# Kernel tuning notes

Measured on AMD Instinct MI355X. Metric: run time of the kernel, lower is better.

## Reference

```python
import jax, jax.numpy as jnp
import numpy as np

N = 100000
E = 1600000
D_IN, D_HID, D_OUT = 256, 256, 128


def _sage_conv(x, src, dst, Wl, bl, Wr, n_nodes):
    # PyG SAGEConv (aggr='mean'): out = lin_l(mean_{j in N(i)} x_j) + lin_r(x_i)
    msg = x[src]                                               # [E, d]
    summed = jax.ops.segment_sum(msg, dst, num_segments=n_nodes)  # [N, d]
    deg = jax.ops.segment_sum(jnp.ones((src.shape[0],), x.dtype), dst,
                              num_segments=n_nodes)            # [N]
    agg = summed / jnp.maximum(deg, 1.0)[:, None]              # mean, 0 if isolated
    return agg @ Wl.T + bl + x @ Wr.T


def setup_inputs() -> dict:
    key = jax.random.key(0)
    ks = jax.random.split(key, 8)
    x = jax.random.normal(ks[0], (N, D_IN), dtype=jnp.float32)
    edge_index = jax.random.randint(ks[1], (2, E), 0, N, dtype=jnp.int32)
    s1 = 1.0 / np.sqrt(D_IN)
    s2 = 1.0 / np.sqrt(D_HID)
    W1l = jax.random.uniform(ks[2], (D_HID, D_IN), jnp.float32, -s1, s1)
    b1 = jnp.zeros((D_HID,), jnp.float32)
    W1r = jax.random.uniform(ks[3], (D_HID, D_IN), jnp.float32, -s1, s1)
    W2l = jax.random.uniform(ks[4], (D_OUT, D_HID), jnp.float32, -s2, s2)
    b2 = jnp.zeros((D_OUT,), jnp.float32)
    W2r = jax.random.uniform(ks[5], (D_OUT, D_HID), jnp.float32, -s2, s2)
    return {"x": x, "edge_index": edge_index, "W1l": W1l, "b1": b1,
            "W1r": W1r, "W2l": W2l, "b2": b2, "W2r": W2r}


def reference(x, edge_index, W1l, b1, W1r, W2l, b2, W2r):
    src, dst = edge_index[0], edge_index[1]
    h = _sage_conv(x, src, dst, W1l, b1, W1r, x.shape[0])
    h = jax.nn.relu(h)
    out = _sage_conv(h, src, dst, W2l, b2, W2r, x.shape[0])
    return out
```

## Files before the change

kernel.cpp:

```cpp
#include <hip/hip_runtime.h>

#define DK 256
#define BN 256
#define NBLK 512

typedef __attribute__((ext_vector_type(8))) short bf16x8;
typedef __attribute__((ext_vector_type(4))) float f32x4;

__device__ __forceinline__ unsigned short f2b(float f) {
    unsigned u = __builtin_bit_cast(unsigned, f);
    u += 0x7FFFu + ((u >> 16) & 1u);
    return (unsigned short)(u >> 16);
}
__device__ __forceinline__ float b2f(unsigned short s) {
    return __builtin_bit_cast(float, (unsigned)s << 16);
}
__device__ __forceinline__ void gld_lds16(void* lds, const void* g) {
    __builtin_amdgcn_global_load_lds(
        (const __attribute__((address_space(1))) unsigned int*)g,
        (__attribute__((address_space(3))) unsigned int*)lds, 16, 0, 0);
}

__global__ __launch_bounds__(256) void k_cvt(const float* __restrict__ src,
                                             unsigned short* __restrict__ dst, int n4) {
    int i = blockIdx.x * 256 + threadIdx.x;
    if (i < n4) {
        float4 v = reinterpret_cast<const float4*>(src)[i];
        ushort4 o = make_ushort4(f2b(v.x), f2b(v.y), f2b(v.z), f2b(v.w));
        reinterpret_cast<ushort4*>(dst)[i] = o;
    }
}

__global__ __launch_bounds__(256) void k_cvtw(const float* __restrict__ a,
                                              const float* __restrict__ b,
                                              const float* __restrict__ c,
                                              const float* __restrict__ d,
                                              unsigned short* __restrict__ Wb1,
                                              unsigned short* __restrict__ Wb2) {
    int i = blockIdx.x * 256 + threadIdx.x;
    const float* s;
    unsigned short* o;
    if (i < 16384)      { s = a; o = Wb1; }
    else if (i < 32768) { s = b; o = Wb1 + 256 * 256; i -= 16384; }
    else if (i < 40960) { s = c; o = Wb2;             i -= 32768; }
    else                { s = d; o = Wb2 + 128 * 256; i -= 40960; }
    float4 v = reinterpret_cast<const float4*>(s)[i];
    ushort4 w = make_ushort4(f2b(v.x), f2b(v.y), f2b(v.z), f2b(v.w));
    reinterpret_cast<ushort4*>(o)[i] = w;
}

__global__ __launch_bounds__(256) void k_scan_a(const int* __restrict__ in,
                                                int* __restrict__ bsum, int N) {
    __shared__ int sm[256];
    int t = threadIdx.x;
    int i0 = blockIdx.x * 1024 + t * 4;
    int s = 0;
    if (i0 + 3 < N) {
        int4 v = *reinterpret_cast<const int4*>(in + i0);
        s = v.x + v.y + v.z + v.w;
    } else {
        for (int i = i0; i < min(i0 + 4, N); ++i) s += in[i];
    }
    sm[t] = s;
    __syncthreads();
    for (int off = 128; off > 0; off >>= 1) {
        if (t < off) sm[t] += sm[t + off];
        __syncthreads();
    }
    if (t == 0) bsum[blockIdx.x] = sm[0];
}

__global__ __launch_bounds__(256) void k_scan_b(const int* __restrict__ bsum,
                                                int* __restrict__ boff,
                                                int* __restrict__ totN, int NB) {
    __shared__ int sm[256];
    int t = threadIdx.x;
    sm[t] = (t < NB) ? bsum[t] : 0;
    __syncthreads();
    for (int off = 1; off < 256; off <<= 1) {
        int v = (t >= off) ? sm[t - off] : 0;
        __syncthreads();
        sm[t] += v;
        __syncthreads();
    }
    if (t < NB) boff[t] = (t == 0) ? 0 : sm[t - 1];
    if (t == NB - 1) *totN = sm[t];
}

__global__ __launch_bounds__(256) void k_scan_c(const int* __restrict__ in,
                                                const int* __restrict__ boff,
                                                int* __restrict__ rowptr,
                                                float* __restrict__ invdeg, int N) {
    __shared__ int sm[256];
    int t = threadIdx.x;
    int i0 = blockIdx.x * 1024 + t * 4;
    int d0 = 0, d1 = 0, d2 = 0, d3 = 0;
    if (i0 + 3 < N) {
        int4 v = *reinterpret_cast<const int4*>(in + i0);
        d0 = v.x; d1 = v.y; d2 = v.z; d3 = v.w;
    } else {
        if (i0 + 0 < N) d0 = in[i0 + 0];
        if (i0 + 1 < N) d1 = in[i0 + 1];
        if (i0 + 2 < N) d2 = in[i0 + 2];
        if (i0 + 3 < N) d3 = in[i0 + 3];
    }
    int s = d0 + d1 + d2 + d3;
    sm[t] = s;
    __syncthreads();
    for (int off = 1; off < 256; off <<= 1) {
        int v = (t >= off) ? sm[t - off] : 0;
        __syncthreads();
        sm[t] += v;
        __syncthreads();
    }
    int run = boff[blockIdx.x] + sm[t] - s;
    int dd[4] = {d0, d1, d2, d3};
#pragma unroll
    for (int i = 0; i < 4; ++i) {
        int idx = i0 + i;
        if (idx < N) {
            rowptr[idx] = run;
            invdeg[idx] = 1.0f / fmaxf((float)dd[i], 1.0f);
            run += dd[i];
        }
    }
}

__global__ __launch_bounds__(256) void k_scan_c2(const int* __restrict__ in,
                                                 const int* __restrict__ boff,
                                                 int* __restrict__ outx, int N) {
    __shared__ int sm[256];
    int t = threadIdx.x;
    int i0 = blockIdx.x * 1024 + t * 4;
    int d0 = 0, d1 = 0, d2 = 0, d3 = 0;
    if (i0 + 3 < N) {
        int4 v = *reinterpret_cast<const int4*>(in + i0);
        d0 = v.x; d1 = v.y; d2 = v.z; d3 = v.w;
    } else {
        if (i0 + 0 < N) d0 = in[i0 + 0];
        if (i0 + 1 < N) d1 = in[i0 + 1];
        if (i0 + 2 < N) d2 = in[i0 + 2];
        if (i0 + 3 < N) d3 = in[i0 + 3];
    }
    int s = d0 + d1 + d2 + d3;
    sm[t] = s;
    __syncthreads();
    for (int off = 1; off < 256; off <<= 1) {
        int v = (t >= off) ? sm[t - off] : 0;
        __syncthreads();
        sm[t] += v;
        __syncthreads();
    }
    int run = boff[blockIdx.x] + sm[t] - s;
    int dd[4] = {d0, d1, d2, d3};
#pragma unroll
    for (int i = 0; i < 4; ++i) {
        int idx = i0 + i;
        if (idx < N) { outx[idx] = run; run += dd[i]; }
    }
}

__global__ __launch_bounds__(256) void k_hist(const int* __restrict__ dst,
                                              int* __restrict__ hist,
                                              int E, int NBUK) {
    extern __shared__ int h[];
    int t = threadIdx.x;
    for (int b = t; b < NBUK; b += 256) h[b] = 0;
    __syncthreads();
    int CH = (E + NBLK - 1) / NBLK;
    int beg = blockIdx.x * CH;
    int end = min(beg + CH, E);
    for (int i = beg + t; i < end; i += 256)
        atomicAdd(&h[dst[i] >> 8], 1);
    __syncthreads();
    for (int b = t; b < NBUK; b += 256)
        hist[b * NBLK + blockIdx.x] = h[b];
}

__global__ __launch_bounds__(256) void k_part(const int* __restrict__ src,
                                              const int* __restrict__ dst,
                                              const int* __restrict__ hoff,
                                              unsigned* __restrict__ scratch,
                                              int E, int NBUK) {
    extern __shared__ int cur[];
    int t = threadIdx.x;
    for (int b = t; b < NBUK; b += 256) cur[b] = hoff[b * NBLK + blockIdx.x];
    __syncthreads();
    int CH = (E + NBLK - 1) / NBLK;
    int beg = blockIdx.x * CH;
    int end = min(beg + CH, E);
    for (int i = beg + t; i < end; i += 256) {
        int d = dst[i];
        int p = atomicAdd(&cur[d >> 8], 1);
        scratch[p] = (unsigned)src[i] | ((unsigned)(d & 255) << 20);
    }
}

__global__ __launch_bounds__(256) void k_degb(const unsigned* __restrict__ scratch,
                                              const int* __restrict__ hoff,
                                              int* __restrict__ degi,
                                              int E, int NBUK, int N) {
    __shared__ int cnt[BN];
    int b = blockIdx.x;
    int t = threadIdx.x;
    cnt[t] = 0;
    __syncthreads();
    int beg = hoff[b * NBLK];
    int end = (b + 1 < NBUK) ? hoff[(b + 1) * NBLK] : E;
    for (int i = beg + t; i < end; i += 256)
        atomicAdd(&cnt[scratch[i] >> 20], 1);
    __syncthreads();
    int node = b * BN + t;
    if (node < N) degi[node] = cnt[t];
}

__global__ __launch_bounds__(256) void k_scatter2(const unsigned* __restrict__ scratch,
                                                  const int* __restrict__ hoff,
                                                  const int* __restrict__ rowptr,
                                                  int* __restrict__ col,
                                                  int E, int NBUK, int N) {
    __shared__ int cur[BN];
    int b = blockIdx.x;
    int t = threadIdx.x;
    int node = b * BN + t;
    if (node < N) cur[t] = rowptr[node];
    __syncthreads();
    int beg = hoff[b * NBLK];
    int end = (b + 1 < NBUK) ? hoff[(b + 1) * NBLK] : E;
    for (int i = beg + t; i < end; i += 256) {
        unsigned v = scratch[i];
        int p = atomicAdd(&cur[v >> 20], 1);
        col[p] = (int)(v & 0xFFFFFu);
    }
}

template <bool RF32, int NT>
__global__ __launch_bounds__(256) void k_gemm_bf16(const unsigned short* __restrict__ A,
                                                   const unsigned short* __restrict__ W,
                                                   unsigned short* __restrict__ Y,
                                                   void* __restrict__ Rv, int N) {
    constexpr int DOUTA = NT * 64;
    __shared__ unsigned short As[128 * 32];
    __shared__ unsigned short Bs[128 * 32];
    const int tid  = threadIdx.x;
    const int lane = tid & 63;
    const int w    = tid >> 6;
    const int wm   = w & 1, wn = w >> 1;
    const int m0   = blockIdx.x * 128;
    const int lm   = lane & 15, quad = lane >> 4;

    const int srow  = lane >> 2;
    const int skoff = (lane & 3) * 8;
    const int ca = 2 * w, cb = 2 * w + 1;

    for (int nt = 0; nt < NT; ++nt) {
        const int n0 = nt * 128;
        f32x4 acc[4][4];
#pragma unroll
        for (int i = 0; i < 4; ++i)
#pragma unroll
            for (int j = 0; j < 4; ++j) acc[i][j] = (f32x4){0.f, 0.f, 0.f, 0.f};

        for (int k0 = 0; k0 < DK; k0 += 32) {
            int ra = min(m0 + 16 * ca + srow, N - 1);
            int rb = min(m0 + 16 * cb + srow, N - 1);
            gld_lds16(As + ca * 512, A + (size_t)ra * DK + k0 + skoff);
            gld_lds16(As + cb * 512, A + (size_t)rb * DK + k0 + skoff);
            int na = n0 + 16 * ca + srow;
            int nb = n0 + 16 * cb + srow;
            gld_lds16(Bs + ca * 512, W + (size_t)na * DK + k0 + skoff);
            gld_lds16(Bs + cb * 512, W + (size_t)nb * DK + k0 + skoff);
            __syncthreads();

            bf16x8 af[4], bfr[4];
#pragma unroll
            for (int mt = 0; mt < 4; ++mt)
                af[mt] = *reinterpret_cast<const bf16x8*>(As + (wm * 64 + mt * 16 + lm) * 32 + quad * 8);
#pragma unroll
            for (int ntf = 0; ntf < 4; ++ntf)
                bfr[ntf] = *reinterpret_cast<const bf16x8*>(Bs + (wn * 64 + ntf * 16 + lm) * 32 + quad * 8);
#pragma unroll
            for (int mt = 0; mt < 4; ++mt)
#pragma unroll
                for (int ntf = 0; ntf < 4; ++ntf)
                    acc[mt][ntf] = __builtin_amdgcn_mfma_f32_16x16x32_bf16(af[mt], bfr[ntf], acc[mt][ntf], 0, 0, 0);
            __syncthreads();
        }

        const bool yPart = (n0 < DOUTA);
#pragma unroll
        for (int mt = 0; mt < 4; ++mt) {
#pragma unroll
            for (int ntf = 0; ntf < 4; ++ntf) {
                int gn = n0 + wn * 64 + ntf * 16 + lm;
#pragma unroll
                for (int reg = 0; reg < 4; ++reg) {
                    int gm = m0 + wm * 64 + mt * 16 + quad * 4 + reg;
                    if (gm < N) {
                        float v = acc[mt][ntf][reg];
                        if (yPart) {
                            Y[(size_t)gm * DOUTA + gn] = f2b(v);
                        } else if (RF32) {
                            ((float*)Rv)[(size_t)gm * DOUTA + (gn - DOUTA)] = v;
                        } else {
                            ((unsigned short*)Rv)[(size_t)gm * DOUTA + (gn - DOUTA)] = f2b(v);
                        }
                    }
                }
            }
        }
    }
}

__global__ __launch_bounds__(256) void k_agg256(const unsigned short* __restrict__ Y,
                                                const unsigned short* __restrict__ Rb,
                                                const float* __restrict__ bias,
                                                const float* __restrict__ invdeg,
                                                const int* __restrict__ rowptr,
                                                const int* __restrict__ col,
                                                unsigned short* __restrict__ H, int N) {
    int g = blockIdx.x * 256 + threadIdx.x;
    int node = g >> 6;
    int lane = g & 63;
    if (node >= N) return;
    int half = lane >> 5, sub = lane & 31;
    int beg = rowptr[node], end = rowptr[node + 1];
    const unsigned short* yb = Y + sub * 8;
    float a[8];
#pragma unroll
    for (int j = 0; j < 8; ++j) a[j] = 0.f;
    int e = beg;
    for (; e + 7 < end; e += 8) {
        int s[4];
#pragma unroll
        for (int u = 0; u < 4; ++u) s[u] = col[e + 2 * u + half];
        bf16x8 v[4];
#pragma unroll
        for (int u = 0; u < 4; ++u)
            v[u] = *reinterpret_cast<const bf16x8*>(yb + (size_t)s[u] * 256);
#pragma unroll
        for (int u = 0; u < 4; ++u)
#pragma unroll
            for (int j = 0; j < 8; ++j) a[j] += b2f((unsigned short)v[u][j]);
    }
    for (; e + 1 < end; e += 2) {
        int s0 = col[e + half];
        bf16x8 v0 = *reinterpret_cast<const bf16x8*>(yb + (size_t)s0 * 256);
#pragma unroll
        for (int j = 0; j < 8; ++j) a[j] += b2f((unsigned short)v0[j]);
    }
    if (e < end && half == 0) {
        int s0 = col[e];
        bf16x8 v0 = *reinterpret_cast<const bf16x8*>(yb + (size_t)s0 * 256);
#pragma unroll
        for (int j = 0; j < 8; ++j) a[j] += b2f((unsigned short)v0[j]);
    }
#pragma unroll
    for (int j = 0; j < 8; ++j) a[j] += __shfl_xor(a[j], 32);
    if (half == 0) {
        float inv = invdeg[node];
        int c = sub * 8;
        bf16x8 r = *reinterpret_cast<const bf16x8*>(Rb + (size_t)node * 256 + c);
        f32x4 b0 = *reinterpret_cast<const f32x4*>(bias + c);
        f32x4 b1v = *reinterpret_cast<const f32x4*>(bias + c + 4);
        bf16x8 o;
#pragma unroll
        for (int j = 0; j < 8; ++j) {
            float bj = (j < 4) ? b0[j] : b1v[j - 4];
            float ov = fmaxf(a[j] * inv + bj + b2f((unsigned short)r[j]), 0.f);
            o[j] = (short)f2b(ov);
        }
        *reinterpret_cast<bf16x8*>(H + (size_t)node * 256 + c) = o;
    }
}

__global__ __launch_bounds__(256) void k_agg128(const unsigned short* __restrict__ Y,
                                                const float* __restrict__ Rf,
                                                const float* __restrict__ bias,
                                                const float* __restrict__ invdeg,
                                                const int* __restrict__ rowptr,
                                                const int* __restrict__ col,
                                                float* __restrict__ O, int N) {
    int g = blockIdx.x * 256 + threadIdx.x;
    int node = g >> 6;
    int lane = g & 63;
    if (node >= N) return;
    int half = lane >> 5, sub = lane & 31;
    int beg = rowptr[node], end = rowptr[node + 1];
    const unsigned short* yb = Y + sub * 4;
    float a0 = 0, a1 = 0, a2 = 0, a3 = 0;
    int e = beg;
    for (; e + 7 < end; e += 8) {
        int s[4];
#pragma unroll
        for (int u = 0; u < 4; ++u) s[u] = col[e + 2 * u + half];
        ushort4 v[4];
#pragma unroll
        for (int u = 0; u < 4; ++u)
            v[u] = *reinterpret_cast<const ushort4*>(yb + (size_t)s[u] * 128);
#pragma unroll
        for (int u = 0; u < 4; ++u) {
            a0 += b2f(v[u].x); a1 += b2f(v[u].y);
            a2 += b2f(v[u].z); a3 += b2f(v[u].w);
        }
    }
    for (; e + 1 < end; e += 2) {
        int s0 = col[e + half];
        ushort4 v0 = *reinterpret_cast<const ushort4*>(yb + (size_t)s0 * 128);
        a0 += b2f(v0.x); a1 += b2f(v0.y); a2 += b2f(v0.z); a3 += b2f(v0.w);
    }
    if (e < end && half == 0) {
        int s0 = col[e];
        ushort4 v0 = *reinterpret_cast<const ushort4*>(yb + (size_t)s0 * 128);
        a0 += b2f(v0.x); a1 += b2f(v0.y); a2 += b2f(v0.z); a3 += b2f(v0.w);
    }
    a0 += __shfl_xor(a0, 32);
    a1 += __shfl_xor(a1, 32);
    a2 += __shfl_xor(a2, 32);
    a3 += __shfl_xor(a3, 32);
    if (half == 0) {
        float inv = invdeg[node];
        int c = sub * 4;
        f32x4 r = *reinterpret_cast<const f32x4*>(Rf + (size_t)node * 128 + c);
        f32x4 bv = *reinterpret_cast<const f32x4*>(bias + c);
        f32x4 o;
        o[0] = a0 * inv + bv[0] + r[0];
        o[1] = a1 * inv + bv[1] + r[1];
        o[2] = a2 * inv + bv[2] + r[2];
        o[3] = a3 * inv + bv[3] + r[3];
        *reinterpret_cast<f32x4*>(O + (size_t)node * 128 + c) = o;
    }
}

extern "C" void kernel_launch(void* const* d_in, const int* in_sizes, int n_in,
                              void* d_out, int out_size, void* d_ws, size_t ws_size,
                              hipStream_t stream) {
    const float* x   = (const float*)d_in[0];
    const int*   ei  = (const int*)d_in[1];
    const float* W1l = (const float*)d_in[2];
    const float* b1  = (const float*)d_in[3];
    const float* W1r = (const float*)d_in[4];
    const float* W2l = (const float*)d_in[5];
    const float* b2  = (const float*)d_in[6];
    const float* W2r = (const float*)d_in[7];
    float* out = (float*)d_out;

    const int N = in_sizes[0] / DK;
    const int E = in_sizes[1] / 2;
    const int* src = ei;
    const int* dst = ei + E;

    unsigned short* xb  = (unsigned short*)d_ws;
    unsigned short* y1b = xb + (size_t)N * 256;
    unsigned short* r1b = y1b + (size_t)N * 256;
    unsigned short* hb  = r1b + (size_t)N * 256;
    unsigned short* Wb1 = hb + (size_t)N * 256;
    unsigned short* Wb2 = Wb1 + 512 * 256;
    float* invdeg = (float*)(Wb2 + 256 * 256);
    int* degi   = (int*)(invdeg + N);
    int* rowptr = degi + N;
    int* col    = rowptr + (N + 1);
    int* bsum   = col + E;
    int* boff   = bsum + 512;
    unsigned short* y2b = y1b;
    float* r2f = (float*)r1b;

    const int NBUK = (N + BN - 1) / BN;
    const int NH   = NBUK * NBLK;
    unsigned* scratch = (unsigned*)hb;
    int* hist  = (int*)y1b;
    int* hoff  = hist + NH;
    int* bsum2 = hoff + NH;
    int* boff2 = bsum2 + 512;
    int* tot2  = boff2 + 512;

    k_cvt<<<(N * 64 + 255) / 256, 256, 0, stream>>>(x, xb, N * 64);
    k_cvtw<<<192, 256, 0, stream>>>(W1l, W1r, W2l, W2r, Wb1, Wb2);

    const int NB2 = (NH + 1023) / 1024;
    const int NB  = (N + 1023) / 1024;
    k_hist<<<NBLK, 256, NBUK * sizeof(int), stream>>>(dst, hist, E, NBUK);
    k_scan_a<<<NB2, 256, 0, stream>>>(hist, bsum2, NH);
    k_scan_b<<<1, 256, 0, stream>>>(bsum2, boff2, tot2, NB2);
    k_scan_c2<<<NB2, 256, 0, stream>>>(hist, boff2, hoff, NH);
    k_part<<<NBLK, 256, NBUK * sizeof(int), stream>>>(src, dst, hoff, scratch, E, NBUK);
    k_degb<<<NBUK, 256, 0, stream>>>(scratch, hoff, degi, E, NBUK, N);
    k_scan_a<<<NB, 256, 0, stream>>>(degi, bsum, N);
    k_scan_b<<<1, 256, 0, stream>>>(bsum, boff, rowptr + N, NB);
    k_scan_c<<<NB, 256, 0, stream>>>(degi, boff, rowptr, invdeg, N);
    k_scatter2<<<NBUK, 256, 0, stream>>>(scratch, hoff, rowptr, col, E, NBUK, N);

    int mTiles = (N + 127) / 128;
    int aggBlocks = (N + 3) / 4;

    k_gemm_bf16<false, 4><<<mTiles, 256, 0, stream>>>(xb, Wb1, y1b, r1b, N);
    k_agg256<<<aggBlocks, 256, 0, stream>>>(y1b, r1b, b1, invdeg, rowptr, col, hb, N);

    k_gemm_bf16<true, 2><<<mTiles, 256, 0, stream>>>(hb, Wb2, y2b, r2f, N);
    k_agg128<<<aggBlocks, 256, 0, stream>>>(y2b, r2f, b2, invdeg, rowptr, col, out, N);
}
```

Measured before the change: 541.7 us.

## Fuse x bf16 conversion into GEMM1 and fuse layer-1 aggregation with GEMM2

The separate fp32-to-bf16 pass over x is removed. The first GEMM now loads fp32 x directly, converts it in registers and writes the result to LDS. The layer-1 aggregation and the second GEMM are merged into one kernel: each block aggregates 64 nodes into an LDS tile of H, then multiplies that tile by W2 with MFMA. This avoids writing H to global memory and reading it back, but W2 fragments are now read straight from global without LDS staging, and each wave aggregates its 16 nodes one after another, which may reduce latency hiding in the gather.

```diff
diff --git a/kernel.cpp b/kernel.cpp
--- a/kernel.cpp
+++ b/kernel.cpp
@@ -19,16 +19,6 @@
     __builtin_amdgcn_global_load_lds(
         (const __attribute__((address_space(1))) unsigned int*)g,
         (__attribute__((address_space(3))) unsigned int*)lds, 16, 0, 0);
-}
-
-__global__ __launch_bounds__(256) void k_cvt(const float* __restrict__ src,
-                                             unsigned short* __restrict__ dst, int n4) {
-    int i = blockIdx.x * 256 + threadIdx.x;
-    if (i < n4) {
-        float4 v = reinterpret_cast<const float4*>(src)[i];
-        ushort4 o = make_ushort4(f2b(v.x), f2b(v.y), f2b(v.z), f2b(v.w));
-        reinterpret_cast<ushort4*>(dst)[i] = o;
-    }
 }
 
 __global__ __launch_bounds__(256) void k_cvtw(const float* __restrict__ a,
@@ -234,12 +224,10 @@
     }
 }
 
-template <bool RF32, int NT>
-__global__ __launch_bounds__(256) void k_gemm_bf16(const unsigned short* __restrict__ A,
-                                                   const unsigned short* __restrict__ W,
-                                                   unsigned short* __restrict__ Y,
-                                                   void* __restrict__ Rv, int N) {
-    constexpr int DOUTA = NT * 64;
+__global__ __launch_bounds__(256) void k_gemm1(const float* __restrict__ X,
+                                               const unsigned short* __restrict__ W,
+                                               unsigned short* __restrict__ Y,
+                                               unsigned short* __restrict__ Rb, int N) {
     __shared__ unsigned short As[128 * 32];
     __shared__ unsigned short Bs[128 * 32];
     const int tid  = threadIdx.x;
@@ -249,11 +237,15 @@
     const int m0   = blockIdx.x * 128;
     const int lm   = lane & 15, quad = lane >> 4;
 
+    const int arow = tid >> 1;
+    const int ako  = (tid & 1) * 16;
+    const float* ap = X + (size_t)min(m0 + arow, N - 1) * 256 + ako;
+
     const int srow  = lane >> 2;
     const int skoff = (lane & 3) * 8;
     const int ca = 2 * w, cb = 2 * w + 1;
 
-    for (int nt = 0; nt < NT; ++nt) {
+    for (int nt = 0; nt < 4; ++nt) {
         const int n0 = nt * 128;
         f32x4 acc[4][4];
 #pragma unroll
@@ -262,14 +254,22 @@
             for (int j = 0; j < 4; ++j) acc[i][j] = (f32x4){0.f, 0.f, 0.f, 0.f};
 
         for (int k0 = 0; k0 < DK; k0 += 32) {
-            int ra = min(m0 + 16 * ca + srow, N - 1);
-            int rb = min(m0 + 16 * cb + srow, N - 1);
-            gld_lds16(As + ca * 512, A + (size_t)ra * DK + k0 + skoff);
-            gld_lds16(As + cb * 512, A + (size_t)rb * DK + k0 + skoff);
-            int na = n0 + 16 * ca + srow;
-            int nb = n0 + 16 * cb + srow;
-            gld_lds16(Bs + ca * 512, W + (size_t)na * DK + k0 + skoff);
-            gld_lds16(Bs + cb * 512, W + (size_t)nb * DK + k0 + skoff);
+            gld_lds16(Bs + ca * 512, W + (size_t)(n0 + 16 * ca + srow) * DK + k0 + skoff);
+            gld_lds16(Bs + cb * 512, W + (size_t)(n0 + 16 * cb + srow) * DK + k0 + skoff);
+            f32x4 x0 = *reinterpret_cast<const f32x4*>(ap + k0);
+            f32x4 x1 = *reinterpret_cast<const f32x4*>(ap + k0 + 4);
+            f32x4 x2 = *reinterpret_cast<const f32x4*>(ap + k0 + 8);
+            f32x4 x3 = *reinterpret_cast<const f32x4*>(ap + k0 + 12);
+            bf16x8 pa, pb;
+#pragma unroll
+            for (int j = 0; j < 4; ++j) {
+                pa[j]     = (short)f2b(x0[j]);
+                pa[4 + j] = (short)f2b(x1[j]);
+                pb[j]     = (short)f2b(x2[j]);
+                pb[4 + j] = (short)f2b(x3[j]);
+            }
+            *reinterpret_cast<bf16x8*>(As + arow * 32 + ako)     = pa;
+            *reinterpret_cast<bf16x8*>(As + arow * 32 + ako + 8) = pb;
             __syncthreads();
 
             bf16x8 af[4], bfr[4];
@@ -287,7 +287,7 @@
             __syncthreads();
         }
 
-        const bool yPart = (n0 < DOUTA);
+        const bool yPart = (n0 < 256);
 #pragma unroll
         for (int mt = 0; mt < 4; ++mt) {
 #pragma unroll
@@ -297,14 +297,9 @@
                 for (int reg = 0; reg < 4; ++reg) {
                     int gm = m0 + wm * 64 + mt * 16 + quad * 4 + reg;
                     if (gm < N) {
-                        float v = acc[mt][ntf][reg];
-                        if (yPart) {
-                            Y[(size_t)gm * DOUTA + gn] = f2b(v);
-                        } else if (RF32) {
-                            ((float*)Rv)[(size_t)gm * DOUTA + (gn - DOUTA)] = v;
-                        } else {
-                            ((unsigned short*)Rv)[(size_t)gm * DOUTA + (gn - DOUTA)] = f2b(v);
-                        }
+                        unsigned short v = f2b(acc[mt][ntf][reg]);
+                        if (yPart) Y[(size_t)gm * 256 + gn] = v;
+                        else       Rb[(size_t)gm * 256 + (gn - 256)] = v;
                     }
                 }
             }
@@ -312,65 +307,125 @@
     }
 }
 
-__global__ __launch_bounds__(256) void k_agg256(const unsigned short* __restrict__ Y,
-                                                const unsigned short* __restrict__ Rb,
-                                                const float* __restrict__ bias,
-                                                const float* __restrict__ invdeg,
-                                                const int* __restrict__ rowptr,
-                                                const int* __restrict__ col,
-                                                unsigned short* __restrict__ H, int N) {
-    int g = blockIdx.x * 256 + threadIdx.x;
-    int node = g >> 6;
-    int lane = g & 63;
-    if (node >= N) return;
-    int half = lane >> 5, sub = lane & 31;
-    int beg = rowptr[node], end = rowptr[node + 1];
+#define HP 264
+__global__ __launch_bounds__(256) void k_aggemm2(const unsigned short* __restrict__ Y,
+                                                 const unsigned short* __restrict__ Rb,
+                                                 const float* __restrict__ bias,
+                                                 const float* __restrict__ invdeg,
+                                                 const int* __restrict__ rowptr,
+                                                 const int* __restrict__ col,
+                                                 const unsigned short* __restrict__ W,
+                                                 unsigned short* __restrict__ Y2,
+                                                 float* __restrict__ R2, int N) {
+    __shared__ unsigned short Hs[64 * HP];
+    const int tid  = threadIdx.x;
+    const int lane = tid & 63;
+    const int w    = tid >> 6;
+    const int nb0  = blockIdx.x * 64;
+    const int half = lane >> 5, sub = lane & 31;
+
     const unsigned short* yb = Y + sub * 8;
-    float a[8];
-#pragma unroll
-    for (int j = 0; j < 8; ++j) a[j] = 0.f;
-    int e = beg;
-    for (; e + 7 < end; e += 8) {
-        int s[4];
-#pragma unroll
-        for (int u = 0; u < 4; ++u) s[u] = col[e + 2 * u + half];
-        bf16x8 v[4];
-#pragma unroll
-        for (int u = 0; u < 4; ++u)
-            v[u] = *reinterpret_cast<const bf16x8*>(yb + (size_t)s[u] * 256);
-#pragma unroll
-        for (int u = 0; u < 4; ++u)
-#pragma unroll
-            for (int j = 0; j < 8; ++j) a[j] += b2f((unsigned short)v[u][j]);
-    }
-    for (; e + 1 < end; e += 2) {
-        int s0 = col[e + half];
-        bf16x8 v0 = *reinterpret_cast<const bf16x8*>(yb + (size_t)s0 * 256);
-#pragma unroll
-        for (int j = 0; j < 8; ++j) a[j] += b2f((unsigned short)v0[j]);
-    }
-    if (e < end && half == 0) {
-        int s0 = col[e];
-        bf16x8 v0 = *reinterpret_cast<const bf16x8*>(yb + (size_t)s0 * 256);
-#pragma unroll
-        for (int j = 0; j < 8; ++j) a[j] += b2f((unsigned short)v0[j]);
-    }
-#pragma unroll
-    for (int j = 0; j < 8; ++j) a[j] += __shfl_xor(a[j], 32);
-    if (half == 0) {
-        float inv = invdeg[node];
-        int c = sub * 8;
-        bf16x8 r = *reinterpret_cast<const bf16x8*>(Rb + (size_t)node * 256 + c);
-        f32x4 b0 = *reinterpret_cast<const f32x4*>(bias + c);
-        f32x4 b1v = *reinterpret_cast<const f32x4*>(bias + c + 4);
-        bf16x8 o;
-#pragma unroll
-        for (int j = 0; j < 8; ++j) {
-            float bj = (j < 4) ? b0[j] : b1v[j - 4];
-            float ov = fmaxf(a[j] * inv + bj + b2f((unsigned short)r[j]), 0.f);
-            o[j] = (short)f2b(ov);
-        }
-        *reinterpret_cast<bf16x8*>(H + (size_t)node * 256 + c) = o;
+    for (int i = 0; i < 16; ++i) {
+        int nl = w * 16 + i;
+        int node = nb0 + nl;
+        if (node >= N) {
+            if (half == 0) {
+                bf16x8 z = {0, 0, 0, 0, 0, 0, 0, 0};
+                *reinterpret_cast<bf16x8*>(Hs + nl * HP + sub * 8) = z;
+            }
+            continue;
+        }
+        int beg = rowptr[node], end = rowptr[node + 1];
+        float a[8];
+#pragma unroll
+        for (int j = 0; j < 8; ++j) a[j] = 0.f;
+        int e = beg;
+        for (; e + 7 < end; e += 8) {
+            int s[4];
+#pragma unroll
+            for (int u = 0; u < 4; ++u) s[u] = col[e + 2 * u + half];
+            bf16x8 v[4];
+#pragma unroll
+            for (int u = 0; u < 4; ++u)
+                v[u] = *reinterpret_cast<const bf16x8*>(yb + (size_t)s[u] * 256);
+#pragma unroll
+            for (int u = 0; u < 4; ++u)
+#pragma unroll
+                for (int j = 0; j < 8; ++j) a[j] += b2f((unsigned short)v[u][j]);
+        }
+        for (; e + 1 < end; e += 2) {
+            int s0 = col[e + half];
+            bf16x8 v0 = *reinterpret_cast<const bf16x8*>(yb + (size_t)s0 * 256);
+#pragma unroll
+            for (int j = 0; j < 8; ++j) a[j] += b2f((unsigned short)v0[j]);
+        }
+        if (e < end && half == 0) {
+            int s0 = col[e];
+            bf16x8 v0 = *reinterpret_cast<const bf16x8*>(yb + (size_t)s0 * 256);
+#pragma unroll
+            for (int j = 0; j < 8; ++j) a[j] += b2f((unsigned short)v0[j]);
+        }
+#pragma unroll
+        for (int j = 0; j < 8; ++j) a[j] += __shfl_xor(a[j], 32);
+        if (half == 0) {
+            float inv = invdeg[node];
+            int c = sub * 8;
+            bf16x8 r = *reinterpret_cast<const bf16x8*>(Rb + (size_t)node * 256 + c);
+            f32x4 b0 = *reinterpret_cast<const f32x4*>(bias + c);
+            f32x4 b1v = *reinterpret_cast<const f32x4*>(bias + c + 4);
+            bf16x8 o;
+#pragma unroll
+            for (int j = 0; j < 8; ++j) {
+                float bj = (j < 4) ? b0[j] : b1v[j - 4];
+                float ov = fmaxf(a[j] * inv + bj + b2f((unsigned short)r[j]), 0.f);
+                o[j] = (short)f2b(ov);
+            }
+            *reinterpret_cast<bf16x8*>(Hs + nl * HP + c) = o;
+        }
+    }
+    __syncthreads();
+
+    const int wm = w & 1, wn = w >> 1;
+    const int lm = lane & 15, quad = lane >> 4;
+    for (int nt = 0; nt < 2; ++nt) {
+        f32x4 acc[2][4];
+#pragma unroll
+        for (int i = 0; i < 2; ++i)
+#pragma unroll
+            for (int j = 0; j < 4; ++j) acc[i][j] = (f32x4){0.f, 0.f, 0.f, 0.f};
+#pragma unroll
+        for (int k0 = 0; k0 < DK; k0 += 32) {
+            bf16x8 af[2], bfr[4];
+#pragma unroll
+            for (int mt = 0; mt < 2; ++mt)
+                af[mt] = *reinterpret_cast<const bf16x8*>(Hs + (wm * 32 + mt * 16 + lm) * HP + k0 + quad * 8);
+#pragma unroll
+            for (int ntf = 0; ntf < 4; ++ntf) {
+                int wr = nt * 128 + wn * 64 + ntf * 16 + lm;
+                bfr[ntf] = *reinterpret_cast<const bf16x8*>(W + (size_t)wr * 256 + k0 + quad * 8);
+            }
+#pragma unroll
+            for (int mt = 0; mt < 2; ++mt)
+#pragma unroll
+                for (int ntf = 0; ntf < 4; ++ntf)
+                    acc[mt][ntf] = __builtin_amdgcn_mfma_f32_16x16x32_bf16(af[mt], bfr[ntf], acc[mt][ntf], 0, 0, 0);
+        }
+#pragma unroll
+        for (int mt = 0; mt < 2; ++mt) {
+#pragma unroll
+            for (int ntf = 0; ntf < 4; ++ntf) {
+                int gn = wn * 64 + ntf * 16 + lm;
+#pragma unroll
+                for (int reg = 0; reg < 4; ++reg) {
+                    int gm = nb0 + wm * 32 + mt * 16 + quad * 4 + reg;
+                    if (gm < N) {
+                        float v = acc[mt][ntf][reg];
+                        if (nt == 0) Y2[(size_t)gm * 128 + gn] = f2b(v);
+                        else         R2[(size_t)gm * 128 + gn] = v;
+                    }
+                }
+            }
+        }
     }
 }
 
@@ -462,8 +517,8 @@
     int* col    = rowptr + (N + 1);
     int* bsum   = col + E;
     int* boff   = bsum + 512;
-    unsigned short* y2b = y1b;
-    float* r2f = (float*)r1b;
+    unsigned short* y2b = hb;
+    float* r2f = (float*)xb;
 
     const int NBUK = (N + BN - 1) / BN;
     const int NH   = NBUK * NBLK;
@@ -474,7 +529,6 @@
     int* boff2 = bsum2 + 512;
     int* tot2  = boff2 + 512;
 
-    k_cvt<<<(N * 64 + 255) / 256, 256, 0, stream>>>(x, xb, N * 64);
     k_cvtw<<<192, 256, 0, stream>>>(W1l, W1r, W2l, W2r, Wb1, Wb2);
 
     const int NB2 = (NH + 1023) / 1024;
@@ -490,12 +544,14 @@
     k_scan_c<<<NB, 256, 0, stream>>>(degi, boff, rowptr, invdeg, N);
     k_scatter2<<<NBUK, 256, 0, stream>>>(scratch, hoff, rowptr, col, E, NBUK, N);
 
-    int mTiles = (N + 127) / 128;
+    int mTiles  = (N + 127) / 128;
+    int fTiles  = (N + 63) / 64;
     int aggBlocks = (N + 3) / 4;
 
-    k_gemm_bf16<false, 4><<<mTiles, 256, 0, stream>>>(xb, Wb1, y1b, r1b, N);
-    k_agg256<<<aggBlocks, 256, 0, stream>>>(y1b, r1b, b1, invdeg, rowptr, col, hb, N);
-
-    k_gemm_bf16<true, 2><<<mTiles, 256, 0, stream>>>(hb, Wb2, y2b, r2f, N);
+    k_gemm1<<<mTiles, 256, 0, stream>>>(x, Wb1, y1b, r1b, N);
+
+    k_aggemm2<<<fTiles, 256, 0, stream>>>(y1b, r1b, b1, invdeg, rowptr, col,
+                                          Wb2, y2b, r2f, N);
+
     k_agg128<<<aggBlocks, 256, 0, stream>>>(y2b, r2f, b2, invdeg, rowptr, col, out, N);
 }
```

Measured after the change: 673.5 us. +24.3%, slower.

## Fuse degree count, row-pointer scan and CSR scatter into one per-bucket kernel

Applied to the files above, without the earlier changes.

Each 256-node bucket's edges already form a contiguous range in the partitioned scratch buffer, so a node's row offset is the bucket start plus a local prefix sum of its degree. The degree histogram, local scan, rowptr/invdeg write and column scatter are merged into one kernel. This removes four launches (degb, scan_a, scan_b, scan_c) and the degree array's global round trip. In exchange the scratch range is read twice within the fused kernel and an in-block scan is added.

```diff
diff --git a/kernel.cpp b/kernel.cpp
--- a/kernel.cpp
+++ b/kernel.cpp
@@ -87,45 +87,6 @@
     if (t == NB - 1) *totN = sm[t];
 }
 
-__global__ __launch_bounds__(256) void k_scan_c(const int* __restrict__ in,
-                                                const int* __restrict__ boff,
-                                                int* __restrict__ rowptr,
-                                                float* __restrict__ invdeg, int N) {
-    __shared__ int sm[256];
-    int t = threadIdx.x;
-    int i0 = blockIdx.x * 1024 + t * 4;
-    int d0 = 0, d1 = 0, d2 = 0, d3 = 0;
-    if (i0 + 3 < N) {
-        int4 v = *reinterpret_cast<const int4*>(in + i0);
-        d0 = v.x; d1 = v.y; d2 = v.z; d3 = v.w;
-    } else {
-        if (i0 + 0 < N) d0 = in[i0 + 0];
-        if (i0 + 1 < N) d1 = in[i0 + 1];
-        if (i0 + 2 < N) d2 = in[i0 + 2];
-        if (i0 + 3 < N) d3 = in[i0 + 3];
-    }
-    int s = d0 + d1 + d2 + d3;
-    sm[t] = s;
-    __syncthreads();
-    for (int off = 1; off < 256; off <<= 1) {
-        int v = (t >= off) ? sm[t - off] : 0;
-        __syncthreads();
-        sm[t] += v;
-        __syncthreads();
-    }
-    int run = boff[blockIdx.x] + sm[t] - s;
-    int dd[4] = {d0, d1, d2, d3};
-#pragma unroll
-    for (int i = 0; i < 4; ++i) {
-        int idx = i0 + i;
-        if (idx < N) {
-            rowptr[idx] = run;
-            invdeg[idx] = 1.0f / fmaxf((float)dd[i], 1.0f);
-            run += dd[i];
-        }
-    }
-}
-
 __global__ __launch_bounds__(256) void k_scan_c2(const int* __restrict__ in,
                                                  const int* __restrict__ boff,
                                                  int* __restrict__ outx, int N) {
@@ -196,13 +157,16 @@
     }
 }
 
-__global__ __launch_bounds__(256) void k_degb(const unsigned* __restrict__ scratch,
-                                              const int* __restrict__ hoff,
-                                              int* __restrict__ degi,
-                                              int E, int NBUK, int N) {
+__global__ __launch_bounds__(256) void k_scatter3(const unsigned* __restrict__ scratch,
+                                                  const int* __restrict__ hoff,
+                                                  int* __restrict__ rowptr,
+                                                  float* __restrict__ invdeg,
+                                                  int* __restrict__ col,
+                                                  int E, int NBUK, int N) {
     __shared__ int cnt[BN];
-    int b = blockIdx.x;
-    int t = threadIdx.x;
+    __shared__ int sm[256];
+    __shared__ int cur[BN];
+    int b = blockIdx.x, t = threadIdx.x;
     cnt[t] = 0;
     __syncthreads();
     int beg = hoff[b * NBLK];
@@ -210,27 +174,28 @@
     for (int i = beg + t; i < end; i += 256)
         atomicAdd(&cnt[scratch[i] >> 20], 1);
     __syncthreads();
+    int v = cnt[t];
+    sm[t] = v;
+    __syncthreads();
+    for (int off = 1; off < 256; off <<= 1) {
+        int u = (t >= off) ? sm[t - off] : 0;
+        __syncthreads();
+        sm[t] += u;
+        __syncthreads();
+    }
     int node = b * BN + t;
-    if (node < N) degi[node] = cnt[t];
-}
-
-__global__ __launch_bounds__(256) void k_scatter2(const unsigned* __restrict__ scratch,
-                                                  const int* __restrict__ hoff,
-                                                  const int* __restrict__ rowptr,
-                                                  int* __restrict__ col,
-                                                  int E, int NBUK, int N) {
-    __shared__ int cur[BN];
-    int b = blockIdx.x;
-    int t = threadIdx.x;
-    int node = b * BN + t;
-    if (node < N) cur[t] = rowptr[node];
-    __syncthreads();
-    int beg = hoff[b * NBLK];
-    int end = (b + 1 < NBUK) ? hoff[(b + 1) * NBLK] : E;
+    if (node < N) {
+        int start = beg + sm[t] - v;
+        rowptr[node] = start;
+        cur[t] = start;
+        invdeg[node] = 1.0f / fmaxf((float)v, 1.0f);
+    }
+    if (b == 0 && t == 0) rowptr[N] = E;
+    __syncthreads();
     for (int i = beg + t; i < end; i += 256) {
-        unsigned v = scratch[i];
-        int p = atomicAdd(&cur[v >> 20], 1);
-        col[p] = (int)(v & 0xFFFFFu);
+        unsigned s = scratch[i];
+        int p = atomicAdd(&cur[s >> 20], 1);
+        col[p] = (int)(s & 0xFFFFFu);
     }
 }
 
@@ -457,8 +422,7 @@
     unsigned short* Wb1 = hb + (size_t)N * 256;
     unsigned short* Wb2 = Wb1 + 512 * 256;
     float* invdeg = (float*)(Wb2 + 256 * 256);
-    int* degi   = (int*)(invdeg + N);
-    int* rowptr = degi + N;
+    int* rowptr = (int*)(invdeg + N);
     int* col    = rowptr + (N + 1);
     int* bsum   = col + E;
     int* boff   = bsum + 512;
@@ -470,25 +434,18 @@
     unsigned* scratch = (unsigned*)hb;
     int* hist  = (int*)y1b;
     int* hoff  = hist + NH;
-    int* bsum2 = hoff + NH;
-    int* boff2 = bsum2 + 512;
-    int* tot2  = boff2 + 512;
+    int* tot2  = boff + 512;
 
     k_cvt<<<(N * 64 + 255) / 256, 256, 0, stream>>>(x, xb, N * 64);
     k_cvtw<<<192, 256, 0, stream>>>(W1l, W1r, W2l, W2r, Wb1, Wb2);
 
     const int NB2 = (NH + 1023) / 1024;
-    const int NB  = (N + 1023) / 1024;
     k_hist<<<NBLK, 256, NBUK * sizeof(int), stream>>>(dst, hist, E, NBUK);
-    k_scan_a<<<NB2, 256, 0, stream>>>(hist, bsum2, NH);
-    k_scan_b<<<1, 256, 0, stream>>>(bsum2, boff2, tot2, NB2);
-    k_scan_c2<<<NB2, 256, 0, stream>>>(hist, boff2, hoff, NH);
+    k_scan_a<<<NB2, 256, 0, stream>>>(hist, bsum, NH);
+    k_scan_b<<<1, 256, 0, stream>>>(bsum, boff, tot2, NB2);
+    k_scan_c2<<<NB2, 256, 0, stream>>>(hist, boff, hoff, NH);
     k_part<<<NBLK, 256, NBUK * sizeof(int), stream>>>(src, dst, hoff, scratch, E, NBUK);
-    k_degb<<<NBUK, 256, 0, stream>>>(scratch, hoff, degi, E, NBUK, N);
-    k_scan_a<<<NB, 256, 0, stream>>>(degi, bsum, N);
-    k_scan_b<<<1, 256, 0, stream>>>(bsum, boff, rowptr + N, NB);
-    k_scan_c<<<NB, 256, 0, stream>>>(degi, boff, rowptr, invdeg, N);
-    k_scatter2<<<NBUK, 256, 0, stream>>>(scratch, hoff, rowptr, col, E, NBUK, N);
+    k_scatter3<<<NBUK, 256, 0, stream>>>(scratch, hoff, rowptr, invdeg, col, E, NBUK, N);
 
     int mTiles = (N + 127) / 128;
     int aggBlocks = (N + 3) / 4;
```

New measurement: 533.5 us. Within noise of the previous version (-1.5%).
